# Kernel optimization log

Measured on AMD Instinct MI355X. Metric: run time of the kernel, lower is better.

The kernel has to match this reference:

```python
import jax, jax.numpy as jnp
import numpy as np

N_WIRES = 8
DIM = 2 ** N_WIRES  # 256
N_OPS = 20

# Fixed realization of tq.RandomLayer(n_ops=20): ops drawn once with a fixed seed.
_rs = np.random.RandomState(0)
RAND_OPS = []
for _ in range(N_OPS):
    k = int(_rs.randint(4))
    if k == 3:
        c, t = _rs.choice(N_WIRES, 2, replace=False)
        RAND_OPS.append(("cnot", int(c), int(t)))
    else:
        RAND_OPS.append((("rx", "ry", "rz")[k], int(_rs.randint(N_WIRES)), 0))

_idx = np.arange(DIM)
# Z eigenvalue sign per wire per basis state (wire 0 = most significant bit)
ZSIGN_NP = np.stack([1.0 - 2.0 * ((_idx >> (N_WIRES - 1 - w)) & 1) for w in range(N_WIRES)]).astype(np.float32)
ZSIGN = jnp.asarray(ZSIGN_NP)        # [8, 256]
ZS_T = jnp.asarray(ZSIGN_NP.T)       # [256, 8]

# CNOT is a basis permutation: precompute index maps for each cnot op.
PERMS = {}
for _i, _op in enumerate(RAND_OPS):
    if _op[0] == "cnot":
        _c, _t = _op[1], _op[2]
        _cb = (_idx >> (N_WIRES - 1 - _c)) & 1
        PERMS[_i] = jnp.asarray(_idx ^ (_cb << (N_WIRES - 1 - _t)))


def _ry_mat(t):
    c = jnp.cos(t * 0.5).astype(jnp.complex64)
    s = jnp.sin(t * 0.5).astype(jnp.complex64)
    return jnp.stack([jnp.stack([c, -s]), jnp.stack([s, c])])


def _rx_mat(t):
    c = jnp.cos(t * 0.5).astype(jnp.complex64)
    s = (-1j * jnp.sin(t * 0.5)).astype(jnp.complex64)
    return jnp.stack([jnp.stack([c, s]), jnp.stack([s, c])])


def _apply_1q(state, U, w):
    # state: [B, 256]; apply 2x2 U on wire w
    B = state.shape[0]
    s = state.reshape(B, 2 ** w, 2, -1)
    return jnp.einsum('ij,bajc->baic', U, s).reshape(B, DIM)


def _forward(x, ry_theta, rand_params, W1, b1, W2, b2):
    B, S, E = x.shape
    f = x.reshape(B * S, E)[:, :N_WIRES]  # encoder uses input_idx 0..7
    # Encoder: RY(f_w) on |0> for each wire -> product state, built by kron chain
    c = jnp.cos(f * 0.5)
    s = jnp.sin(f * 0.5)
    state = jnp.ones((B * S, 1), jnp.float32)
    for w in range(N_WIRES):
        v = jnp.stack([c[:, w], s[:, w]], axis=-1)  # [BS, 2]
        state = (state[:, :, None] * v[:, None, :]).reshape(B * S, -1)
    state = state.astype(jnp.complex64)  # [BS, 256]
    # Fixed random layer
    for i, op in enumerate(RAND_OPS):
        kind = op[0]
        if kind == "cnot":
            state = state[:, PERMS[i]]
        elif kind == "rz":
            ph = jnp.exp((-0.5j * rand_params[i]) * ZSIGN[op[1]]).astype(jnp.complex64)
            state = state * ph[None, :]
        elif kind == "rx":
            state = _apply_1q(state, _rx_mat(rand_params[i]), op[1])
        else:
            state = _apply_1q(state, _ry_mat(rand_params[i]), op[1])
    # Trainable per-wire RY gates
    for w in range(N_WIRES):
        state = _apply_1q(state, _ry_mat(ry_theta[w]), w)
    # MeasureAll(PauliZ): <Z_w> = sum_b |amp_b|^2 * zsign_w(b)
    probs = (state.real ** 2 + state.imag ** 2)  # [BS, 256] float32
    expv = probs @ ZS_T                          # [BS, 8]
    h = jax.nn.relu(expv @ W1.T + b1)
    out = h @ W2.T + b2
    return out.reshape(B, S, -1)


def setup_inputs() -> dict:
    key = jax.random.key(0)
    k1, k2, k3, k4, k5 = jax.random.split(key, 5)
    B, S, E = 4, 4096, 512
    pi = 3.14159265
    x = jax.random.normal(k1, (B, S, E), jnp.float32)
    ry_theta = jax.random.uniform(k2, (N_WIRES,), jnp.float32, -pi, pi)
    rand_params = jax.random.uniform(k3, (N_OPS,), jnp.float32, -pi, pi)
    W1 = jax.random.normal(k4, (64, N_WIRES), jnp.float32) * (1.0 / np.sqrt(N_WIRES))
    b1 = jnp.zeros((64,), jnp.float32)
    W2 = jax.random.normal(k5, (E, 64), jnp.float32) * (1.0 / 8.0)
    b2 = jnp.zeros((E,), jnp.float32)
    return {"x": x, "ry_theta": ry_theta, "rand_params": rand_params, "W1": W1, "b1": b1, "W2": W2, "b2": b2}


def reference(x, ry_theta, rand_params, W1, b1, W2, b2):
    return _forward(x, ry_theta, rand_params, W1, b1, W2, b2)
```

## Files before the change

kernel.cpp:

```cpp
#include <hip/hip_runtime.h>
#include <hip/hip_fp16.h>
#include <cstdint>

#define N_RAND   20
#define N_GATES  28
#define E_DIM    512

struct OpsArg { int d[N_GATES]; };

struct MT19937ce {
  uint32_t mt[624] = {};
  int mti = 0;
  constexpr void seed(uint32_t s){
    mt[0]=s;
    for(int i=1;i<624;i++) mt[i]=1812433253u*(mt[i-1]^(mt[i-1]>>30))+(uint32_t)i;
    mti=624;
  }
  constexpr uint32_t next(){
    if(mti>=624){
      for(int i=0;i<624;i++){
        uint32_t y=(mt[i]&0x80000000u)|(mt[(i+1)%624]&0x7fffffffu);
        mt[i]=mt[(i+397)%624]^(y>>1)^((y&1u)?0x9908b0dfu:0u);
      }
      mti=0;
    }
    uint32_t y=mt[mti++];
    y^=y>>11; y^=(y<<7)&0x9d2c5680u; y^=(y<<15)&0xefc60000u; y^=y>>18;
    return y;
  }
  constexpr uint32_t interval(uint32_t mx){
    if(!mx) return 0;
    uint32_t mask=mx; mask|=mask>>1; mask|=mask>>2; mask|=mask>>4; mask|=mask>>8; mask|=mask>>16;
    uint32_t v = next()&mask;
    while(v>mx) v = next()&mask;
    return v;
  }
};

constexpr OpsArg build_ops_ce(){
  MT19937ce rs; rs.seed(0);
  OpsArg o{};
  for(int i=0;i<N_RAND;i++){
    uint32_t k = rs.interval(3);
    if(k==3){
      int perm[8] = {0,1,2,3,4,5,6,7};
      for(int j=7;j>=1;j--){
        uint32_t t=rs.interval((uint32_t)j);
        int tmp=perm[j]; perm[j]=perm[t]; perm[t]=tmp;
      }
      o.d[i] = 3 | (perm[0]<<2) | (perm[1]<<5);
    } else {
      uint32_t w = rs.interval(7);
      o.d[i] = (int)k | ((int)w<<2);
    }
  }
  for(int i=0;i<8;i++) o.d[N_RAND+i] = 1 | (i<<2);
  return o;
}
inline constexpr OpsArg OPS = build_ops_ce();

__device__ __forceinline__ float readlane_f(float v, int l){
  return __int_as_float(__builtin_amdgcn_readlane(__float_as_int(v), l));
}
template<int CTRL>
__device__ __forceinline__ float dpp_mov(float v){
  int s = __float_as_int(v);
  return __int_as_float(__builtin_amdgcn_update_dpp(s, s, CTRL, 0xF, 0xF, false));
}
template<int M>
__device__ __forceinline__ float xl(float v){
  if constexpr (M==1)      return dpp_mov<0xB1>(v);
  else if constexpr (M==2) return dpp_mov<0x4E>(v);
  else return __int_as_float(__builtin_amdgcn_ds_swizzle(__float_as_int(v), (M<<10)|0x1F));
}
template<int L>
__device__ __forceinline__ float bcast(float v){
  return __int_as_float(__builtin_amdgcn_ds_swizzle(__float_as_int(v), L<<5));
}

typedef _Float16 v2h __attribute__((ext_vector_type(2)));
typedef _Float16 v8h __attribute__((ext_vector_type(8)));
typedef float    v4f __attribute__((ext_vector_type(4)));
union HU  { uint32_t u; v2h h; };

template<int G>
__device__ __forceinline__ void run_gates(float (&ar)[8], float (&ai)[8],
                                          const float (&sgn)[5], int l,
                                          float cv, float sv)
{
  if constexpr (G < N_GATES){
    constexpr int dd   = OPS.d[G];
    constexpr int kind = dd & 3;
    constexpr int wa   = (dd>>2) & 7;
    constexpr int wb   = (dd>>5) & 7;
    const float gc = readlane_f(cv, G);
    const float gs = readlane_f(sv, G);

    if constexpr (kind == 3){
      if constexpr (wa < 3 && wb < 3){
        constexpr int Rc = 4>>wa, Rt = 4>>wb;
        #pragma unroll
        for (int r=0;r<8;r++){
          if ((r & Rc) && !(r & Rt)){
            float t0=ar[r]; ar[r]=ar[r|Rt]; ar[r|Rt]=t0;
            float t1=ai[r]; ai[r]=ai[r|Rt]; ai[r|Rt]=t1;
          }
        }
      } else if constexpr (wa < 3){
        constexpr int Rc = 4>>wa, Mt = 16>>(wb-3);
        #pragma unroll
        for (int r=0;r<8;r++){
          if (r & Rc){ ar[r]=xl<Mt>(ar[r]); ai[r]=xl<Mt>(ai[r]); }
        }
      } else if constexpr (wb < 3){
        constexpr int Mc = 16>>(wa-3), Rt = 4>>wb;
        const bool cb = (l & Mc) != 0;
        #pragma unroll
        for (int r=0;r<8;r++){
          if (!(r & Rt)){
            float alo=ar[r], ahi=ar[r|Rt];
            ar[r]    = cb ? ahi : alo;  ar[r|Rt] = cb ? alo : ahi;
            float blo=ai[r], bhi=ai[r|Rt];
            ai[r]    = cb ? bhi : blo;  ai[r|Rt] = cb ? blo : bhi;
          }
        }
      } else {
        constexpr int Mc = 16>>(wa-3), Mt = 16>>(wb-3);
        const bool cb = (l & Mc) != 0;
        #pragma unroll
        for (int r=0;r<8;r++){
          float pr = xl<Mt>(ar[r]), pi_ = xl<Mt>(ai[r]);
          ar[r] = cb ? pr  : ar[r];
          ai[r] = cb ? pi_ : ai[r];
        }
      }
    } else if constexpr (kind == 2){
      if constexpr (wa < 3){
        constexpr int Rb = 4>>wa;
        #pragma unroll
        for (int r=0;r<8;r++){
          const float pim = (r & Rb) ? gs : -gs;
          float nr = gc*ar[r] - pim*ai[r];
          ai[r] = gc*ai[r] + pim*ar[r];
          ar[r] = nr;
        }
      } else {
        constexpr int SI = wa-3;
        const float pim = sgn[SI]*gs;
        #pragma unroll
        for (int r=0;r<8;r++){
          float nr = gc*ar[r] - pim*ai[r];
          ai[r] = gc*ai[r] + pim*ar[r];
          ar[r] = nr;
        }
      }
    } else if constexpr (kind == 1){
      if constexpr (wa < 3){
        constexpr int Rb = 4>>wa;
        #pragma unroll
        for (int r=0;r<8;r++){
          if (!(r & Rb)){
            const int h = r|Rb;
            float lr=ar[r], li=ai[r], hr=ar[h], hii=ai[h];
            ar[r]=gc*lr - gs*hr;  ai[r]=gc*li - gs*hii;
            ar[h]=gs*lr + gc*hr;  ai[h]=gs*li + gc*hii;
          }
        }
      } else {
        constexpr int M = 16>>(wa-3), SI = wa-3;
        const float sg = sgn[SI]*gs;
        #pragma unroll
        for (int r=0;r<8;r++){
          float pr = xl<M>(ar[r]), pi_ = xl<M>(ai[r]);
          ar[r] = gc*ar[r] + sg*pr;
          ai[r] = gc*ai[r] + sg*pi_;
        }
      }
    } else {
      if constexpr (wa < 3){
        constexpr int Rb = 4>>wa;
        #pragma unroll
        for (int r=0;r<8;r++){
          if (!(r & Rb)){
            const int h = r|Rb;
            float lr=ar[r], li=ai[r], hr=ar[h], hii=ai[h];
            ar[r]=gc*lr + gs*hii;  ai[r]=gc*li - gs*hr;
            ar[h]=gc*hr + gs*li;   ai[h]=gc*hii - gs*lr;
          }
        }
      } else {
        constexpr int M = 16>>(wa-3);
        #pragma unroll
        for (int r=0;r<8;r++){
          float pr = xl<M>(ar[r]), pi_ = xl<M>(ai[r]);
          ar[r] = gc*ar[r] + gs*pi_;
          ai[r] = gc*ai[r] - gs*pr;
        }
      }
    }
    run_gates<G+1>(ar, ai, sgn, l, cv, sv);
  }
}

#define TS_STRIDE 68
#define HPAD 72
__global__ __launch_bounds__(512)
void qffb_fused(const float* __restrict__ x,
                const float* __restrict__ ry_theta,
                const float* __restrict__ rand_params,
                const float* __restrict__ W1,
                const float* __restrict__ b1,
                const float* __restrict__ W2,
                const float* __restrict__ b2,
                float* __restrict__ out)
{
  __shared__ __half Hs[16][HPAD];
  __shared__ float  Ts[8][16*TS_STRIDE];

  const int tid  = threadIdx.x;
  const int lane = tid & 63;
  const int l    = lane & 31;
  const int wave = tid >> 6;
  const int trow = wave*2 + (lane>>5);
  const int token = blockIdx.x*16 + trow;

  float th = 0.f;
  if (lane < N_GATES)
    th = (lane < N_RAND) ? rand_params[lane] : ry_theta[lane - N_RAND];
  float cv, sv;
  __sincosf(0.5f*th, &sv, &cv);

  const float4 xa = *(const float4*)(x + (size_t)token*E_DIM);
  const float4 xb = *(const float4*)(x + (size_t)token*E_DIM + 4);
  float c[8], s[8];
  {
    float xs[8] = {xa.x, xa.y, xa.z, xa.w, xb.x, xb.y, xb.z, xb.w};
    #pragma unroll
    for (int w=0; w<8; ++w) __sincosf(0.5f*xs[w], &s[w], &c[w]);
  }

  float sgn[5];
  sgn[0] = (l&16) ? 1.f : -1.f;
  sgn[1] = (l& 8) ? 1.f : -1.f;
  sgn[2] = (l& 4) ? 1.f : -1.f;
  sgn[3] = (l& 2) ? 1.f : -1.f;
  sgn[4] = (l& 1) ? 1.f : -1.f;

  float lp = ((l&16)? s[3]:c[3]) * ((l&8)? s[4]:c[4]);
  lp *= ((l&4)? s[5]:c[5]) * ((l&2)? s[6]:c[6]);
  lp *= ((l&1)? s[7]:c[7]);
  const float q00=c[0]*c[1], q01=c[0]*s[1], q10=s[0]*c[1], q11=s[0]*s[1];
  const float c2lp=c[2]*lp, s2lp=s[2]*lp;
  float ar[8], ai[8];
  ar[0]=q00*c2lp; ar[1]=q00*s2lp; ar[2]=q01*c2lp; ar[3]=q01*s2lp;
  ar[4]=q10*c2lp; ar[5]=q10*s2lp; ar[6]=q11*c2lp; ar[7]=q11*s2lp;
  #pragma unroll
  for (int r=0;r<8;r++) ai[r]=0.f;

  run_gates<0>(ar, ai, sgn, l, cv, sv);

  float p[8];
  #pragma unroll
  for (int r=0;r<8;r++) p[r] = ar[r]*ar[r] + ai[r]*ai[r];
  const float t1a=p[0]+p[1], t1b=p[2]+p[3], t1c=p[4]+p[5], t1d=p[6]+p[7];
  const float s0a=t1a+t1b, s0b=t1c+t1d;
  float P  = s0a + s0b;
  float e0 = s0a - s0b;
  float e1 = (t1a+t1c) - (t1b+t1d);
  float e2 = (p[0]-p[1])+(p[2]-p[3])+(p[4]-p[5])+(p[6]-p[7]);
  {
    float t;
    t=xl<1>(e0); e0+=t;  t=xl<1>(e1); e1+=t;  t=xl<1>(e2); e2+=t;
    t=xl<1>(P);  P = fmaf(-sgn[4], P, t);
    t=xl<2>(e0); e0+=t;  t=xl<2>(e1); e1+=t;  t=xl<2>(e2); e2+=t;
    t=xl<2>(P);  P = fmaf(-sgn[3], P, t);
    t=xl<4>(e0); e0+=t;  t=xl<4>(e1); e1+=t;  t=xl<4>(e2); e2+=t;
    t=xl<4>(P);  P = fmaf(-sgn[2], P, t);
    t=xl<8>(e0); e0+=t;  t=xl<8>(e1); e1+=t;  t=xl<8>(e2); e2+=t;
    t=xl<8>(P);  P = fmaf(-sgn[1], P, t);
    t=xl<16>(e0); e0+=t; t=xl<16>(e1); e1+=t; t=xl<16>(e2); e2+=t;
    t=xl<16>(P); P = fmaf(-sgn[0], P, t);
  }
  const float e3 = bcast<16>(P);
  const float e4 = bcast<8>(P);
  const float e5 = bcast<4>(P);
  const float e6 = bcast<2>(P);
  const float e7 = bcast<1>(P);

  const float4 wA0 = *(const float4*)(W1 + (size_t)(2*l)*8);
  const float4 wA1 = *(const float4*)(W1 + (size_t)(2*l)*8 + 4);
  const float4 wB0 = *(const float4*)(W1 + (size_t)(2*l+1)*8);
  const float4 wB1 = *(const float4*)(W1 + (size_t)(2*l+1)*8 + 4);
  const float2 bb  = *(const float2*)(b1 + 2*l);
  float h0 = bb.x + wA0.x*e0 + wA0.y*e1 + wA0.z*e2 + wA0.w*e3
                  + wA1.x*e4 + wA1.y*e5 + wA1.z*e6 + wA1.w*e7;
  float h1 = bb.y + wB0.x*e0 + wB0.y*e1 + wB0.z*e2 + wB0.w*e3
                  + wB1.x*e4 + wB1.y*e5 + wB1.z*e6 + wB1.w*e7;
  HU pk;
  pk.h = v2h{(_Float16)fmaxf(h0,0.f), (_Float16)fmaxf(h1,0.f)};
  *(uint32_t*)((char*)&Hs[trow][0] + 4*l) = pk.u;

  __syncthreads();

  const int mt   = blockIdx.x;
  const int ng   = wave;
  const int rr   = lane & 15;
  const int quad = lane >> 4;

  const v8h a0 = *(const v8h*)&Hs[rr][quad*8];
  const v8h a1 = *(const v8h*)&Hs[rr][32 + quad*8];

  #pragma unroll
  for (int j=0;j<4;++j){
    const int e = ng*64 + j*16 + rr;
    const float4 wa = *(const float4*)(W2 + (size_t)e*64 + quad*8);
    const float4 wb = *(const float4*)(W2 + (size_t)e*64 + quad*8 + 4);
    const float4 wc = *(const float4*)(W2 + (size_t)e*64 + 32 + quad*8);
    const float4 wd = *(const float4*)(W2 + (size_t)e*64 + 32 + quad*8 + 4);
    const v8h b0 = v8h{(_Float16)wa.x,(_Float16)wa.y,(_Float16)wa.z,(_Float16)wa.w,
                      (_Float16)wb.x,(_Float16)wb.y,(_Float16)wb.z,(_Float16)wb.w};
    const v8h b1v = v8h{(_Float16)wc.x,(_Float16)wc.y,(_Float16)wc.z,(_Float16)wc.w,
                      (_Float16)wd.x,(_Float16)wd.y,(_Float16)wd.z,(_Float16)wd.w};
    v4f acc = {0.f,0.f,0.f,0.f};
    acc = __builtin_amdgcn_mfma_f32_16x16x32_f16(a0, b0, acc, 0, 0, 0);
    acc = __builtin_amdgcn_mfma_f32_16x16x32_f16(a1, b1v, acc, 0, 0, 0);
    #pragma unroll
    for (int r2=0;r2<4;r2++)
      Ts[wave][(quad*4+r2)*TS_STRIDE + j*16 + rr] = acc[r2];
  }


  const float4 bias = *(const float4*)(b2 + ng*64 + rr*4);
  #pragma unroll
  for (int k=0;k<4;++k){
    const int row = 4*k + quad;
    float4 v = *(const float4*)&Ts[wave][row*TS_STRIDE + rr*4];
    v.x += bias.x; v.y += bias.y; v.z += bias.z; v.w += bias.w;
    const int t = mt*16 + row;
    *(float4*)(out + (size_t)t*E_DIM + ng*64 + rr*4) = v;
  }
}

extern "C" void kernel_launch(void* const* d_in, const int* in_sizes, int n_in,
                              void* d_out, int out_size, void* d_ws, size_t ws_size,
                              hipStream_t stream)
{
  (void)n_in; (void)out_size; (void)d_ws; (void)ws_size;
  const int ntok = in_sizes[0] / E_DIM;

  qffb_fused<<<ntok/16, 512, 0, stream>>>(
      (const float*)d_in[0],
      (const float*)d_in[1],
      (const float*)d_in[2],
      (const float*)d_in[3],
      (const float*)d_in[4],
      (const float*)d_in[5],
      (const float*)d_in[6],
      (float*)d_out);
}
```

Measured before the change: 111.5 us.

## Precompute circuit unitary and apply it via fp16 MFMA matmul

Adds a small pre-kernel that runs the fixed gate sequence on the 256 basis states to build the full 256x256 circuit unitary, stored as fp16 real and imaginary parts in workspace. The main kernel then builds each token's product state, writes it to LDS as fp16, and multiplies it by the unitary with MFMA instead of simulating the gates per token with cross-lane shuffles. Probabilities go through LDS into the existing reduction and MLP. This swaps per-token shuffle-heavy gate work for dense matrix-core work plus a 256 KB unitary read per block, adds a second launch, and loses precision because amplitudes are held in fp16.

```diff
diff --git a/kernel.cpp b/kernel.cpp
--- a/kernel.cpp
+++ b/kernel.cpp
@@ -202,42 +202,23 @@
   }
 }
 
-#define TS_STRIDE 68
-#define HPAD 72
 __global__ __launch_bounds__(512)
-void qffb_fused(const float* __restrict__ x,
-                const float* __restrict__ ry_theta,
-                const float* __restrict__ rand_params,
-                const float* __restrict__ W1,
-                const float* __restrict__ b1,
-                const float* __restrict__ W2,
-                const float* __restrict__ b2,
-                float* __restrict__ out)
+void qffb_pre(const float* __restrict__ ry_theta,
+              const float* __restrict__ rand_params,
+              _Float16* __restrict__ Urh,
+              _Float16* __restrict__ Uih)
 {
-  __shared__ __half Hs[16][HPAD];
-  __shared__ float  Ts[8][16*TS_STRIDE];
-
   const int tid  = threadIdx.x;
   const int lane = tid & 63;
   const int l    = lane & 31;
   const int wave = tid >> 6;
-  const int trow = wave*2 + (lane>>5);
-  const int token = blockIdx.x*16 + trow;
+  const int b    = blockIdx.x*16 + wave*2 + (lane>>5);
 
   float th = 0.f;
   if (lane < N_GATES)
     th = (lane < N_RAND) ? rand_params[lane] : ry_theta[lane - N_RAND];
   float cv, sv;
   __sincosf(0.5f*th, &sv, &cv);
-
-  const float4 xa = *(const float4*)(x + (size_t)token*E_DIM);
-  const float4 xb = *(const float4*)(x + (size_t)token*E_DIM + 4);
-  float c[8], s[8];
-  {
-    float xs[8] = {xa.x, xa.y, xa.z, xa.w, xb.x, xb.y, xb.z, xb.w};
-    #pragma unroll
-    for (int w=0; w<8; ++w) __sincosf(0.5f*xs[w], &s[w], &c[w]);
-  }
 
   float sgn[5];
   sgn[0] = (l&16) ? 1.f : -1.f;
@@ -246,22 +227,104 @@
   sgn[3] = (l& 2) ? 1.f : -1.f;
   sgn[4] = (l& 1) ? 1.f : -1.f;
 
-  float lp = ((l&16)? s[3]:c[3]) * ((l&8)? s[4]:c[4]);
-  lp *= ((l&4)? s[5]:c[5]) * ((l&2)? s[6]:c[6]);
-  lp *= ((l&1)? s[7]:c[7]);
-  const float q00=c[0]*c[1], q01=c[0]*s[1], q10=s[0]*c[1], q11=s[0]*s[1];
-  const float c2lp=c[2]*lp, s2lp=s[2]*lp;
   float ar[8], ai[8];
-  ar[0]=q00*c2lp; ar[1]=q00*s2lp; ar[2]=q01*c2lp; ar[3]=q01*s2lp;
-  ar[4]=q10*c2lp; ar[5]=q10*s2lp; ar[6]=q11*c2lp; ar[7]=q11*s2lp;
-  #pragma unroll
-  for (int r=0;r<8;r++) ai[r]=0.f;
+  #pragma unroll
+  for (int r=0;r<8;r++){
+    ar[r] = (((b>>5)==r) && ((b&31)==l)) ? 1.f : 0.f;
+    ai[r] = 0.f;
+  }
 
   run_gates<0>(ar, ai, sgn, l, cv, sv);
 
+  #pragma unroll
+  for (int r=0;r<8;r++){
+    const int j = r*32 + l;
+    Urh[(size_t)j*256 + b] = (_Float16)ar[r];
+    Uih[(size_t)j*256 + b] = (_Float16)ai[r];
+  }
+}
+
+#define PSTRIDE 272
+#define PFSTR   264
+__global__ __launch_bounds__(512)
+void qffb_main(const float* __restrict__ x,
+               const _Float16* __restrict__ Urh,
+               const _Float16* __restrict__ Uih,
+               const float* __restrict__ W1,
+               const float* __restrict__ b1,
+               const float* __restrict__ W2,
+               const float* __restrict__ b2,
+               float* __restrict__ out)
+{
+  __shared__ _Float16 Ps[16*PSTRIDE];
+  __shared__ _Float16 Hs[16][72];
+  __shared__ float    Ts[8][16*68];
+  float* Pf = &Ts[0][0];
+
+  const int tid  = threadIdx.x;
+  const int lane = tid & 63;
+  const int l    = lane & 31;
+  const int wave = tid >> 6;
+  const int rr   = lane & 15;
+  const int quad = lane >> 4;
+  const int trow = wave*2 + (lane>>5);
+  const int token = blockIdx.x*16 + trow;
+
+  {
+    const float4 xa = *(const float4*)(x + (size_t)token*E_DIM);
+    const float4 xb = *(const float4*)(x + (size_t)token*E_DIM + 4);
+    float c[8], s[8];
+    float xs[8] = {xa.x, xa.y, xa.z, xa.w, xb.x, xb.y, xb.z, xb.w};
+    #pragma unroll
+    for (int w=0; w<8; ++w) __sincosf(0.5f*xs[w], &s[w], &c[w]);
+    float L = ((l&16)? s[0]:c[0]) * ((l&8)? s[1]:c[1]);
+    L *= ((l&4)? s[2]:c[2]) * ((l&2)? s[3]:c[3]);
+    L *= ((l&1)? s[4]:c[4]);
+    const float p67[4] = {c[6]*c[7], c[6]*s[7], s[6]*c[7], s[6]*s[7]};
+    v8h v;
+    #pragma unroll
+    for (int i=0;i<8;++i)
+      v[i] = (_Float16)(L * (((i&4)? s[5]:c[5]) * p67[i&3]));
+    *(v8h*)&Ps[trow*PSTRIDE + l*8] = v;
+  }
+  __syncthreads();
+
+  v4f accr[2], acci[2];
+  #pragma unroll
+  for (int n=0;n<2;++n){ accr[n]=v4f{0.f,0.f,0.f,0.f}; acci[n]=v4f{0.f,0.f,0.f,0.f}; }
+  for (int k=0;k<8;++k){
+    const v8h a0 = *(const v8h*)&Ps[rr*PSTRIDE + k*32 + quad*8];
+    #pragma unroll
+    for (int n=0;n<2;++n){
+      const int nt = wave*2 + n;
+      const size_t boff = ((size_t)(nt*16+rr))*256 + k*32 + quad*8;
+      const v8h br = *(const v8h*)(Urh + boff);
+      const v8h bi = *(const v8h*)(Uih + boff);
+      accr[n] = __builtin_amdgcn_mfma_f32_16x16x32_f16(a0, br, accr[n], 0,0,0);
+      acci[n] = __builtin_amdgcn_mfma_f32_16x16x32_f16(a0, bi, acci[n], 0,0,0);
+    }
+  }
+  #pragma unroll
+  for (int n=0;n<2;++n){
+    const int nt = wave*2 + n;
+    #pragma unroll
+    for (int r2=0;r2<4;++r2)
+      Pf[(quad*4+r2)*PFSTR + nt*16 + rr] =
+          accr[n][r2]*accr[n][r2] + acci[n][r2]*acci[n][r2];
+  }
+  __syncthreads();
+
+  float sgn[5];
+  sgn[0] = (l&16) ? 1.f : -1.f;
+  sgn[1] = (l& 8) ? 1.f : -1.f;
+  sgn[2] = (l& 4) ? 1.f : -1.f;
+  sgn[3] = (l& 2) ? 1.f : -1.f;
+  sgn[4] = (l& 1) ? 1.f : -1.f;
+
   float p[8];
   #pragma unroll
-  for (int r=0;r<8;r++) p[r] = ar[r]*ar[r] + ai[r]*ai[r];
+  for (int r=0;r<8;r++) p[r] = Pf[trow*PFSTR + r*32 + l];
+
   const float t1a=p[0]+p[1], t1b=p[2]+p[3], t1c=p[4]+p[5], t1d=p[6]+p[7];
   const float s0a=t1a+t1b, s0b=t1c+t1d;
   float P  = s0a + s0b;
@@ -287,25 +350,24 @@
   const float e6 = bcast<2>(P);
   const float e7 = bcast<1>(P);
 
-  const float4 wA0 = *(const float4*)(W1 + (size_t)(2*l)*8);
-  const float4 wA1 = *(const float4*)(W1 + (size_t)(2*l)*8 + 4);
-  const float4 wB0 = *(const float4*)(W1 + (size_t)(2*l+1)*8);
-  const float4 wB1 = *(const float4*)(W1 + (size_t)(2*l+1)*8 + 4);
-  const float2 bb  = *(const float2*)(b1 + 2*l);
-  float h0 = bb.x + wA0.x*e0 + wA0.y*e1 + wA0.z*e2 + wA0.w*e3
-                  + wA1.x*e4 + wA1.y*e5 + wA1.z*e6 + wA1.w*e7;
-  float h1 = bb.y + wB0.x*e0 + wB0.y*e1 + wB0.z*e2 + wB0.w*e3
-                  + wB1.x*e4 + wB1.y*e5 + wB1.z*e6 + wB1.w*e7;
-  HU pk;
-  pk.h = v2h{(_Float16)fmaxf(h0,0.f), (_Float16)fmaxf(h1,0.f)};
-  *(uint32_t*)((char*)&Hs[trow][0] + 4*l) = pk.u;
-
+  {
+    const float4 wA0 = *(const float4*)(W1 + (size_t)(2*l)*8);
+    const float4 wA1 = *(const float4*)(W1 + (size_t)(2*l)*8 + 4);
+    const float4 wB0 = *(const float4*)(W1 + (size_t)(2*l+1)*8);
+    const float4 wB1 = *(const float4*)(W1 + (size_t)(2*l+1)*8 + 4);
+    const float2 bb  = *(const float2*)(b1 + 2*l);
+    float h0 = bb.x + wA0.x*e0 + wA0.y*e1 + wA0.z*e2 + wA0.w*e3
+                    + wA1.x*e4 + wA1.y*e5 + wA1.z*e6 + wA1.w*e7;
+    float h1 = bb.y + wB0.x*e0 + wB0.y*e1 + wB0.z*e2 + wB0.w*e3
+                    + wB1.x*e4 + wB1.y*e5 + wB1.z*e6 + wB1.w*e7;
+    HU pk;
+    pk.h = v2h{(_Float16)fmaxf(h0,0.f), (_Float16)fmaxf(h1,0.f)};
+    *(uint32_t*)((char*)&Hs[trow][0] + 4*l) = pk.u;
+  }
   __syncthreads();
 
-  const int mt   = blockIdx.x;
-  const int ng   = wave;
-  const int rr   = lane & 15;
-  const int quad = lane >> 4;
+  const int mt = blockIdx.x;
+  const int ng = wave;
 
   const v8h a0 = *(const v8h*)&Hs[rr][quad*8];
   const v8h a1 = *(const v8h*)&Hs[rr][32 + quad*8];
@@ -326,15 +388,14 @@
     acc = __builtin_amdgcn_mfma_f32_16x16x32_f16(a1, b1v, acc, 0, 0, 0);
     #pragma unroll
     for (int r2=0;r2<4;r2++)
-      Ts[wave][(quad*4+r2)*TS_STRIDE + j*16 + rr] = acc[r2];
-  }
-
+      Ts[wave][(quad*4+r2)*68 + j*16 + rr] = acc[r2];
+  }
 
   const float4 bias = *(const float4*)(b2 + ng*64 + rr*4);
   #pragma unroll
   for (int k=0;k<4;++k){
     const int row = 4*k + quad;
-    float4 v = *(const float4*)&Ts[wave][row*TS_STRIDE + rr*4];
+    float4 v = *(const float4*)&Ts[wave][row*68 + rr*4];
     v.x += bias.x; v.y += bias.y; v.z += bias.z; v.w += bias.w;
     const int t = mt*16 + row;
     *(float4*)(out + (size_t)t*E_DIM + ng*64 + rr*4) = v;
@@ -345,13 +406,20 @@
                               void* d_out, int out_size, void* d_ws, size_t ws_size,
                               hipStream_t stream)
 {
-  (void)n_in; (void)out_size; (void)d_ws; (void)ws_size;
+  (void)n_in; (void)out_size; (void)ws_size;
   const int ntok = in_sizes[0] / E_DIM;
-
-  qffb_fused<<<ntok/16, 512, 0, stream>>>(
-      (const float*)d_in[0],
+  char* ws = (char*)d_ws;
+  _Float16* Urh = (_Float16*)(ws);
+  _Float16* Uih = (_Float16*)(ws + 131072);
+
+  qffb_pre<<<16, 512, 0, stream>>>(
       (const float*)d_in[1],
       (const float*)d_in[2],
+      Urh, Uih);
+
+  qffb_main<<<ntok/16, 512, 0, stream>>>(
+      (const float*)d_in[0],
+      Urh, Uih,
       (const float*)d_in[3],
       (const float*)d_in[4],
       (const float*)d_in[5],
```

After: 143.3 us. +28.5%, slower.
